# Kernel tuning notes

Measured on AMD Instinct MI355X. Metric: run time of the kernel, lower is better.

The kernel has to match this reference:

```python
import jax, jax.numpy as jnp
import numpy as np

BS, S, H, T = 16, 256, 1024, 32  # batch, num entities, hidden, num relation tags
N_TAGS = 7


def setup_inputs() -> dict:
    key = jax.random.key(0)
    k0, k1, k2, k3 = jax.random.split(key, 4)
    seq_embedding = jax.random.normal(k0, (BS, H), dtype=jnp.float32)
    entities_embeddings = jax.random.normal(k1, (BS, S, H), dtype=jnp.float32)
    entities_tags = jax.random.randint(k2, (BS, S), 0, N_TAGS)
    # relation_classifier: Linear(3*H -> T)
    W = jax.random.normal(k3, (T, 3 * H), dtype=jnp.float32) * 0.02
    b = jnp.zeros((T,), dtype=jnp.float32)
    return {
        "seq_embedding": seq_embedding,
        "entities_embeddings": entities_embeddings,
        "W": W,
        "b": b,
        "entities_tags": entities_tags,
    }


def reference(seq_embedding, entities_embeddings, W, b, entities_tags):
    # Original (eval mode, dropout=identity):
    #   pred[b,i,j] = W @ concat(E[b,i], E[b,j], S[b]) + bias
    # (arg1/arg2/all_seq linears and tag embeddings are dead code in the
    #  original forward: their outputs are never used.)
    # Decompose W = [W1 | W2 | W3] along the feature axis; mathematically
    # identical to materializing the (bs,S,S,3H) concat tensor.
    h = entities_embeddings.shape[-1]
    W1, W2, W3 = W[:, :h], W[:, h:2 * h], W[:, 2 * h:]
    p1 = jnp.einsum('bih,th->bit', entities_embeddings, W1)  # arg1 contribution
    p2 = jnp.einsum('bjh,th->bjt', entities_embeddings, W2)  # arg2 contribution
    ps = seq_embedding @ W3.T + b                             # seq + bias
    # (bs, S, S, T)
    return p1[:, :, None, :] + p2[:, None, :, :] + ps[:, None, None, :]
```

## Files before the change

kernel.cpp:

```cpp
#include <hip/hip_runtime.h>

#define BS 16
#define S  256
#define H  1024
#define T  32
#define KSPLIT 4
#define KCH (H / KSPLIT)
#define BM 32

#define PP_OFF 0
#define PP_SZ  (KSPLIT * BS * S * 64)
#define PS_OFF (PP_OFF + PP_SZ)
#define P1_OFF (PS_OFF + 512)
#define P2_OFF (P1_OFF + BS * S * T)

typedef __bf16 bf16x8 __attribute__((ext_vector_type(8)));
typedef float  f32x4  __attribute__((ext_vector_type(4)));

__global__ __launch_bounds__(256) void gemm_partial(
    const float* __restrict__ seq, const float* __restrict__ E,
    const float* __restrict__ W, const float* __restrict__ bias,
    float* __restrict__ ws)
{
    const int tid = threadIdx.x;
    const int lane = tid & 63, wv = tid >> 6;

    if (blockIdx.x >= 512) {
        float* ps = ws + PS_OFF;
        const int o = (blockIdx.x - 512) * 4 + wv;
        const int bb = o >> 5, t = o & 31;
        const float4* sp = (const float4*)(seq + (size_t)bb * H) + lane * 4;
        const float4* wp = (const float4*)(W + (size_t)t * (3 * H) + 2 * H) + lane * 4;
        float acc = 0.f;
        #pragma unroll
        for (int k = 0; k < 4; ++k) {
            float4 a = sp[k], w = wp[k];
            acc += a.x * w.x + a.y * w.y + a.z * w.z + a.w * w.w;
        }
        #pragma unroll
        for (int m = 32; m >= 1; m >>= 1) acc += __shfl_xor(acc, m);
        if (lane == 0) ps[o] = acc + bias[t];
        return;
    }

    __shared__ __align__(16) float Ef[BM][KCH + 4];
    const int ks = blockIdx.x >> 7;
    const int m0 = (blockIdx.x & 127) * BM;
    const int kbeg = ks * KCH;

    const int nb = wv * 16;
    const int wrow = nb + (lane & 15);
    const int ksub = (lane >> 4) * 8;
    const float* wbase = W + (size_t)(wrow & 31) * (3 * H) + ((wrow >> 5) ? H : 0)
                           + kbeg + ksub;
    bf16x8 bfrag[8];
    #pragma unroll
    for (int s = 0; s < 8; ++s) {
        float4 lo = *(const float4*)(wbase + s * 32);
        float4 hi = *(const float4*)(wbase + s * 32 + 4);
        bf16x8 b;
        b[0] = (__bf16)lo.x; b[1] = (__bf16)lo.y; b[2] = (__bf16)lo.z; b[3] = (__bf16)lo.w;
        b[4] = (__bf16)hi.x; b[5] = (__bf16)hi.y; b[6] = (__bf16)hi.z; b[7] = (__bf16)hi.w;
        bfrag[s] = b;
    }

    #pragma unroll
    for (int i = 0; i < 8; ++i) {
        int f = tid + i * 256;
        int row = f >> 6, c4 = f & 63;
        float4 v = *(const float4*)(E + (size_t)(m0 + row) * H + kbeg + c4 * 4);
        *(float4*)&Ef[row][c4 * 4] = v;
    }
    __syncthreads();

    f32x4 acc0 = {0.f, 0.f, 0.f, 0.f}, acc1 = {0.f, 0.f, 0.f, 0.f};
    const int erow = lane & 15;
    #pragma unroll
    for (int s = 0; s < 8; ++s) {
        const float* e0 = &Ef[erow][s * 32 + ksub];
        const float* e1 = &Ef[erow + 16][s * 32 + ksub];
        float4 p = *(const float4*)e0, q = *(const float4*)(e0 + 4);
        float4 r = *(const float4*)e1, u = *(const float4*)(e1 + 4);
        bf16x8 a0, a1;
        a0[0] = (__bf16)p.x; a0[1] = (__bf16)p.y; a0[2] = (__bf16)p.z; a0[3] = (__bf16)p.w;
        a0[4] = (__bf16)q.x; a0[5] = (__bf16)q.y; a0[6] = (__bf16)q.z; a0[7] = (__bf16)q.w;
        a1[0] = (__bf16)r.x; a1[1] = (__bf16)r.y; a1[2] = (__bf16)r.z; a1[3] = (__bf16)r.w;
        a1[4] = (__bf16)u.x; a1[5] = (__bf16)u.y; a1[6] = (__bf16)u.z; a1[7] = (__bf16)u.w;
        acc0 = __builtin_amdgcn_mfma_f32_16x16x32_bf16(a0, bfrag[s], acc0, 0, 0, 0);
        acc1 = __builtin_amdgcn_mfma_f32_16x16x32_bf16(a1, bfrag[s], acc1, 0, 0, 0);
    }

    float* pp = ws + PP_OFF + (size_t)ks * (BS * S * 64);
    const int orow = (lane >> 4) * 4;
    const int ocol = nb + (lane & 15);
    #pragma unroll
    for (int r = 0; r < 4; ++r) {
        pp[(size_t)(m0 + orow + r) * 64 + ocol]      = acc0[r];
        pp[(size_t)(m0 + 16 + orow + r) * 64 + ocol] = acc1[r];
    }
}

__global__ __launch_bounds__(256) void reduce_p(float* __restrict__ ws)
{
    const int o = blockIdx.x * 256 + threadIdx.x;
    const float4* pp = (const float4*)(ws + PP_OFF);
    float4 v = pp[o];
    #pragma unroll
    for (int ks = 1; ks < KSPLIT; ++ks) {
        float4 u = pp[o + ks * (PP_SZ / KSPLIT / 4)];
        v.x += u.x; v.y += u.y; v.z += u.z; v.w += u.w;
    }
    const int row = o >> 4, c4 = o & 15;
    if (c4 < 8) {
        const int b = row >> 8;
        float4 s = ((const float4*)(ws + PS_OFF))[b * 8 + c4];
        v.x += s.x; v.y += s.y; v.z += s.z; v.w += s.w;
        ((float4*)(ws + P1_OFF))[row * 8 + c4] = v;
    } else {
        ((float4*)(ws + P2_OFF))[row * 8 + (c4 - 8)] = v;
    }
}

__global__ __launch_bounds__(256) void bcast_add(
    const float* __restrict__ ws, float* __restrict__ out)
{
    const int blk = blockIdx.x;
    const int b = blk >> 8, i = blk & 255;
    const int tid = threadIdx.x;

    __shared__ __align__(16) float s1[32];
    if (tid < 32) s1[tid] = (ws + P1_OFF)[(size_t)(b * S + i) * T + tid];
    __syncthreads();

    const float4 s = *(const float4*)&s1[(tid & 7) * 4];
    const float4* p2v = (const float4*)(ws + P2_OFF) + (size_t)b * (S * T / 4);
    float4* ov = (float4*)out + (size_t)(b * S + i) * (S * T / 4);

    #pragma unroll
    for (int k = tid; k < S * T / 4; k += 256) {
        float4 v = p2v[k];
        float4 r;
        r.x = v.x + s.x; r.y = v.y + s.y; r.z = v.z + s.z; r.w = v.w + s.w;
        ov[k] = r;
    }
}

extern "C" void kernel_launch(void* const* d_in, const int* in_sizes, int n_in,
                              void* d_out, int out_size, void* d_ws, size_t ws_size,
                              hipStream_t stream)
{
    const float* seq  = (const float*)d_in[0];
    const float* E    = (const float*)d_in[1];
    const float* W    = (const float*)d_in[2];
    const float* bias = (const float*)d_in[3];
    float* out = (float*)d_out;
    float* ws  = (float*)d_ws;

    gemm_partial<<<640, 256, 0, stream>>>(seq, E, W, bias, ws);
    reduce_p<<<256, 256, 0, stream>>>(ws);
    bcast_add<<<BS * S, 256, 0, stream>>>(ws, out);
}
```

Measured before the change: 38.87 us.

## Stage entity tiles as bf16 in LDS and drop shared staging in broadcast

```diff
diff --git a/kernel.cpp b/kernel.cpp
--- a/kernel.cpp
+++ b/kernel.cpp
@@ -5,7 +5,7 @@
 #define H  1024
 #define T  32
 #define KSPLIT 4
-#define KCH (H / KSPLIT)
+#define KCH 256
 #define BM 32
 
 #define PP_OFF 0
@@ -17,7 +17,14 @@
 typedef __bf16 bf16x8 __attribute__((ext_vector_type(8)));
 typedef float  f32x4  __attribute__((ext_vector_type(4)));
 
-__global__ __launch_bounds__(256) void gemm_partial(
+__device__ inline bf16x8 to_bf8(float4 lo, float4 hi) {
+    bf16x8 r;
+    r[0] = (__bf16)lo.x; r[1] = (__bf16)lo.y; r[2] = (__bf16)lo.z; r[3] = (__bf16)lo.w;
+    r[4] = (__bf16)hi.x; r[5] = (__bf16)hi.y; r[6] = (__bf16)hi.z; r[7] = (__bf16)hi.w;
+    return r;
+}
+
+__global__ __launch_bounds__(256) void gemm_ps(
     const float* __restrict__ seq, const float* __restrict__ E,
     const float* __restrict__ W, const float* __restrict__ bias,
     float* __restrict__ ws)
@@ -25,9 +32,9 @@
     const int tid = threadIdx.x;
     const int lane = tid & 63, wv = tid >> 6;
 
-    if (blockIdx.x >= 512) {
+    if (blockIdx.x < 128) {
         float* ps = ws + PS_OFF;
-        const int o = (blockIdx.x - 512) * 4 + wv;
+        const int o = blockIdx.x * 4 + wv;
         const int bb = o >> 5, t = o & 31;
         const float4* sp = (const float4*)(seq + (size_t)bb * H) + lane * 4;
         const float4* wp = (const float4*)(W + (size_t)t * (3 * H) + 2 * H) + lane * 4;
@@ -43,49 +50,40 @@
         return;
     }
 
-    __shared__ __align__(16) float Ef[BM][KCH + 4];
-    const int ks = blockIdx.x >> 7;
-    const int m0 = (blockIdx.x & 127) * BM;
+    __shared__ __align__(16) __bf16 Ebf[BM][280];
+
+    const int g = blockIdx.x - 128;
+    const int ks = g >> 7;
+    const int m0 = (g & 127) * BM;
     const int kbeg = ks * KCH;
 
     const int nb = wv * 16;
     const int wrow = nb + (lane & 15);
     const int ksub = (lane >> 4) * 8;
-    const float* wbase = W + (size_t)(wrow & 31) * (3 * H) + ((wrow >> 5) ? H : 0)
-                           + kbeg + ksub;
+    const float* wbase = W + (size_t)(wrow & 31) * (3 * H)
+                           + ((wrow >> 5) ? H : 0) + kbeg + ksub;
     bf16x8 bfrag[8];
     #pragma unroll
-    for (int s = 0; s < 8; ++s) {
-        float4 lo = *(const float4*)(wbase + s * 32);
-        float4 hi = *(const float4*)(wbase + s * 32 + 4);
-        bf16x8 b;
-        b[0] = (__bf16)lo.x; b[1] = (__bf16)lo.y; b[2] = (__bf16)lo.z; b[3] = (__bf16)lo.w;
-        b[4] = (__bf16)hi.x; b[5] = (__bf16)hi.y; b[6] = (__bf16)hi.z; b[7] = (__bf16)hi.w;
-        bfrag[s] = b;
-    }
+    for (int s = 0; s < 8; ++s)
+        bfrag[s] = to_bf8(*(const float4*)(wbase + s * 32),
+                          *(const float4*)(wbase + s * 32 + 4));
 
     #pragma unroll
-    for (int i = 0; i < 8; ++i) {
+    for (int i = 0; i < 4; ++i) {
         int f = tid + i * 256;
-        int row = f >> 6, c4 = f & 63;
-        float4 v = *(const float4*)(E + (size_t)(m0 + row) * H + kbeg + c4 * 4);
-        *(float4*)&Ef[row][c4 * 4] = v;
+        int row = f >> 5, c8 = f & 31;
+        const float4* src = (const float4*)(E + (size_t)(m0 + row) * H
+                                            + kbeg + c8 * 8);
+        *(bf16x8*)&Ebf[row][c8 * 8] = to_bf8(src[0], src[1]);
     }
     __syncthreads();
 
-    f32x4 acc0 = {0.f, 0.f, 0.f, 0.f}, acc1 = {0.f, 0.f, 0.f, 0.f};
+    f32x4 acc0 = {0.f,0.f,0.f,0.f}, acc1 = {0.f,0.f,0.f,0.f};
     const int erow = lane & 15;
     #pragma unroll
     for (int s = 0; s < 8; ++s) {
-        const float* e0 = &Ef[erow][s * 32 + ksub];
-        const float* e1 = &Ef[erow + 16][s * 32 + ksub];
-        float4 p = *(const float4*)e0, q = *(const float4*)(e0 + 4);
-        float4 r = *(const float4*)e1, u = *(const float4*)(e1 + 4);
-        bf16x8 a0, a1;
-        a0[0] = (__bf16)p.x; a0[1] = (__bf16)p.y; a0[2] = (__bf16)p.z; a0[3] = (__bf16)p.w;
-        a0[4] = (__bf16)q.x; a0[5] = (__bf16)q.y; a0[6] = (__bf16)q.z; a0[7] = (__bf16)q.w;
-        a1[0] = (__bf16)r.x; a1[1] = (__bf16)r.y; a1[2] = (__bf16)r.z; a1[3] = (__bf16)r.w;
-        a1[4] = (__bf16)u.x; a1[5] = (__bf16)u.y; a1[6] = (__bf16)u.z; a1[7] = (__bf16)u.w;
+        bf16x8 a0 = *(const bf16x8*)&Ebf[erow][s * 32 + ksub];
+        bf16x8 a1 = *(const bf16x8*)&Ebf[erow + 16][s * 32 + ksub];
         acc0 = __builtin_amdgcn_mfma_f32_16x16x32_bf16(a0, bfrag[s], acc0, 0, 0, 0);
         acc1 = __builtin_amdgcn_mfma_f32_16x16x32_bf16(a1, bfrag[s], acc1, 0, 0, 0);
     }
@@ -128,11 +126,8 @@
     const int b = blk >> 8, i = blk & 255;
     const int tid = threadIdx.x;
 
-    __shared__ __align__(16) float s1[32];
-    if (tid < 32) s1[tid] = (ws + P1_OFF)[(size_t)(b * S + i) * T + tid];
-    __syncthreads();
-
-    const float4 s = *(const float4*)&s1[(tid & 7) * 4];
+    const float4 s = *(const float4*)((ws + P1_OFF)
+                     + (size_t)(b * S + i) * T + (tid & 7) * 4);
     const float4* p2v = (const float4*)(ws + P2_OFF) + (size_t)b * (S * T / 4);
     float4* ov = (float4*)out + (size_t)(b * S + i) * (S * T / 4);
 
@@ -156,7 +151,7 @@
     float* out = (float*)d_out;
     float* ws  = (float*)d_ws;
 
-    gemm_partial<<<640, 256, 0, stream>>>(seq, E, W, bias, ws);
+    gemm_ps<<<640, 256, 0, stream>>>(seq, E, W, bias, ws);
     reduce_p<<<256, 256, 0, stream>>>(ws);
     bcast_add<<<BS * S, 256, 0, stream>>>(ws, out);
 }
```

New measurement: 37.91 us. -2.5%, faster.
